# Performance work log

Measured on AMD Instinct MI355X. Metric: run time of the kernel, lower is better.

## Reference

```python
import jax, jax.numpy as jnp
import numpy as np

INPUT_DIM, PROJ_DIM, HIDDEN = 1, 16, 32
B, T = 2048, 2048


def setup_inputs() -> dict:
    key = jax.random.key(0)
    ks = jax.random.split(key, 9)
    s_in = 1.0 / np.sqrt(INPUT_DIM)
    s_h = 1.0 / np.sqrt(HIDDEN)
    s_p = 1.0 / np.sqrt(PROJ_DIM)
    return {
        "x_seq": jax.random.normal(ks[0], (B, T, INPUT_DIM), dtype=jnp.float32),
        # input_linear: Linear(input_dim, proj_dim)
        "Wp": jax.random.uniform(ks[1], (PROJ_DIM, INPUT_DIM), minval=-s_in, maxval=s_in),
        "bp": jax.random.uniform(ks[2], (PROJ_DIM,), minval=-s_in, maxval=s_in),
        # LSTM weights (PyTorch gate order i,f,g,o)
        "W_ih": jax.random.uniform(ks[3], (4 * HIDDEN, PROJ_DIM), minval=-s_h, maxval=s_h),
        "W_hh": jax.random.uniform(ks[4], (4 * HIDDEN, HIDDEN), minval=-s_h, maxval=s_h),
        "b_ih": jax.random.uniform(ks[5], (4 * HIDDEN,), minval=-s_h, maxval=s_h),
        "b_hh": jax.random.uniform(ks[6], (4 * HIDDEN,), minval=-s_h, maxval=s_h),
        # output_linear: Linear(hidden, input_dim)
        "Wo": jax.random.uniform(ks[7], (INPUT_DIM, HIDDEN), minval=-s_h, maxval=s_h),
        "bo": jax.random.uniform(ks[8], (INPUT_DIM,), minval=-s_h, maxval=s_h),
    }


def reference(x_seq, Wp, bp, W_ih, W_hh, b_ih, b_hh, Wo, bo):
    H = W_hh.shape[1]
    b, t, _ = x_seq.shape
    # input projection for all timesteps at once (same math as per-step Linear)
    # then pre-apply W_ih: [B,T,4H]
    xp = jnp.einsum("bti,pi->btp", x_seq, Wp) + bp
    gates_x = jnp.einsum("btp,gp->btg", xp, W_ih) + b_ih + b_hh
    gates_x = jnp.transpose(gates_x, (1, 0, 2))  # [T,B,4H]

    def step(carry, gx):
        h, c = carry
        gates = gx + h @ W_hh.T  # [B,4H]
        i, f, g, o = jnp.split(gates, 4, axis=-1)
        i = jax.nn.sigmoid(i)
        f = jax.nn.sigmoid(f)
        g = jnp.tanh(g)
        o = jax.nn.sigmoid(o)
        c = f * c + i * g
        h = o * jnp.tanh(c)
        return (h, c), h

    h0 = jnp.zeros((b, H), dtype=x_seq.dtype)
    c0 = jnp.zeros((b, H), dtype=x_seq.dtype)
    (_, _), hs = jax.lax.scan(step, (h0, c0), gates_x)  # hs: [T,B,H]
    outputs = jnp.einsum("tbh,oh->bto", hs, Wo) + bo  # [B,T,input_dim]
    return outputs
```

## Files before the change

kernel.cpp:

```cpp
#include <hip/hip_runtime.h>


#define BB 2048
#define TT 2048
#define HH 32

typedef _Float16 h2 __attribute__((ext_vector_type(2)));

__device__ __forceinline__ float gate_eval(float x, float m, float a, float b) {
    float e = __builtin_amdgcn_exp2f(x * m);
    float r = __builtin_amdgcn_rcpf(1.0f + e);
    return fmaf(a, r, b);
}

template <int CTRL>
__device__ __forceinline__ float dpp_add(float v) {
    int s = __builtin_amdgcn_update_dpp(0, __float_as_int(v), CTRL, 0xf, 0xf, true);
    return v + __int_as_float(s);
}

struct HVec { h2 v[16]; };

__device__ __forceinline__ HVec gather_h(const _Float16* base) {
    const float4* p = (const float4*)base;
    float4 q0 = p[0], q1 = p[1], q2 = p[2], q3 = p[3];
    HVec r;
    r.v[0]  = __builtin_bit_cast(h2, q0.x); r.v[1]  = __builtin_bit_cast(h2, q0.y);
    r.v[2]  = __builtin_bit_cast(h2, q0.z); r.v[3]  = __builtin_bit_cast(h2, q0.w);
    r.v[4]  = __builtin_bit_cast(h2, q1.x); r.v[5]  = __builtin_bit_cast(h2, q1.y);
    r.v[6]  = __builtin_bit_cast(h2, q1.z); r.v[7]  = __builtin_bit_cast(h2, q1.w);
    r.v[8]  = __builtin_bit_cast(h2, q2.x); r.v[9]  = __builtin_bit_cast(h2, q2.y);
    r.v[10] = __builtin_bit_cast(h2, q2.z); r.v[11] = __builtin_bit_cast(h2, q2.w);
    r.v[12] = __builtin_bit_cast(h2, q3.x); r.v[13] = __builtin_bit_cast(h2, q3.y);
    r.v[14] = __builtin_bit_cast(h2, q3.z); r.v[15] = __builtin_bit_cast(h2, q3.w);
    return r;
}

__global__ __launch_bounds__(256) void lstm_fused_kernel(
    const float* __restrict__ x_seq,
    const float* __restrict__ Wp,
    const float* __restrict__ bp,
    const float* __restrict__ W_ih,
    const float* __restrict__ W_hh,
    const float* __restrict__ b_ih,
    const float* __restrict__ b_hh,
    const float* __restrict__ Wo,
    const float* __restrict__ bo,
    float* __restrict__ out)
{
    const int tid  = threadIdx.x;
    const int wave = tid >> 6;
    const int lane = tid & 63;
    const int half = lane >> 5;
    const int j    = lane & 31;
    const int b    = blockIdx.x * 8 + wave * 2 + half;

    const int rI = j, rF = HH + j, rG = 2 * HH + j, rO = 3 * HH + j;

    h2 wI[16], wF[16], wG[16], wO[16];
    {
        const float2* pI = (const float2*)(W_hh + rI * HH);
        const float2* pF = (const float2*)(W_hh + rF * HH);
        const float2* pG = (const float2*)(W_hh + rG * HH);
        const float2* pO = (const float2*)(W_hh + rO * HH);
#pragma unroll
        for (int k = 0; k < 16; ++k) {
            float2 a = pI[k], f = pF[k], g = pG[k], o = pO[k];
            wI[k].x = (_Float16)a.x; wI[k].y = (_Float16)a.y;
            wF[k].x = (_Float16)f.x; wF[k].y = (_Float16)f.y;
            wG[k].x = (_Float16)g.x; wG[k].y = (_Float16)g.y;
            wO[k].x = (_Float16)o.x; wO[k].y = (_Float16)o.y;
        }
    }

    float aI = 0.f, cI = 0.f, aF = 0.f, cF = 0.f;
    float aG = 0.f, cG = 0.f, aO = 0.f, cO = 0.f;
#pragma unroll
    for (int p = 0; p < 16; ++p) {
        float wpv = Wp[p], bpv = bp[p];
        float wi = W_ih[rI * 16 + p], wf = W_ih[rF * 16 + p];
        float wg = W_ih[rG * 16 + p], wo_ = W_ih[rO * 16 + p];
        aI = fmaf(wi, wpv, aI);  cI = fmaf(wi, bpv, cI);
        aF = fmaf(wf, wpv, aF);  cF = fmaf(wf, bpv, cF);
        aG = fmaf(wg, wpv, aG);  cG = fmaf(wg, bpv, cG);
        aO = fmaf(wo_, wpv, aO); cO = fmaf(wo_, bpv, cO);
    }
    cI += b_ih[rI] + b_hh[rI];
    cF += b_ih[rF] + b_hh[rF];
    cG += b_ih[rG] + b_hh[rG];
    cO += b_ih[rO] + b_hh[rO];

    const float LOG2E = 1.44269504088896340736f;
    const float woj = Wo[j];
    const float bo0 = bo[0];

    __shared__ __align__(16) _Float16 hsh[4][2][HH];
    _Float16* hbase = &hsh[wave][half][0];
    hbase[j] = (_Float16)0.0f;

    float c = 0.0f;
    const float* xp = x_seq + (size_t)b * TT;
    float* op = out + (size_t)b * TT;

    HVec hcur = gather_h(hbase);
    float4 x4 = *(const float4*)(xp);

    for (int t = 0; t < TT; t += 4) {
        const int tn = (t + 4 < TT) ? (t + 4) : t;
        float4 x4n = *(const float4*)(xp + tn);
        float outv[4];
#pragma unroll
        for (int u = 0; u < 4; ++u) {
            float xv = (u == 0) ? x4.x : (u == 1) ? x4.y : (u == 2) ? x4.z : x4.w;

            float sI0 = cI, sI1 = xv * aI;
            float sF0 = cF, sF1 = xv * aF;
            float sG0 = cG, sG1 = xv * aG;
            float sO0 = cO, sO1 = xv * aO;
#pragma unroll
            for (int k = 0; k < 16; k += 2) {
                h2 h0 = hcur.v[k], h1 = hcur.v[k + 1];
                sI0 = __builtin_amdgcn_fdot2(wI[k],     h0, sI0, false);
                sF0 = __builtin_amdgcn_fdot2(wF[k],     h0, sF0, false);
                sG0 = __builtin_amdgcn_fdot2(wG[k],     h0, sG0, false);
                sO0 = __builtin_amdgcn_fdot2(wO[k],     h0, sO0, false);
                sI1 = __builtin_amdgcn_fdot2(wI[k + 1], h1, sI1, false);
                sF1 = __builtin_amdgcn_fdot2(wF[k + 1], h1, sF1, false);
                sG1 = __builtin_amdgcn_fdot2(wG[k + 1], h1, sG1, false);
                sO1 = __builtin_amdgcn_fdot2(wO[k + 1], h1, sO1, false);
            }

            float iv = gate_eval(sI0 + sI1, -LOG2E, 1.0f, 0.0f);
            float fv = gate_eval(sF0 + sF1, -LOG2E, 1.0f, 0.0f);
            float gv = gate_eval(sG0 + sG1, -2.0f * LOG2E, 2.0f, -1.0f);
            float ov = gate_eval(sO0 + sO1, -LOG2E, 1.0f, 0.0f);

            c = fmaf(fv, c, iv * gv);
            float th = gate_eval(c, -2.0f * LOG2E, 2.0f, -1.0f);
            float h = ov * th;

            hbase[j] = (_Float16)h;
            hcur = gather_h(hbase);

            float po = woj * h;
            po = dpp_add<0x111>(po);
            po = dpp_add<0x112>(po);
            po = dpp_add<0x114>(po);
            po = dpp_add<0x118>(po);
            po = dpp_add<0x142>(po);
            outv[u] = po + bo0;
        }
        if ((lane & 31) == 31) {
            *(float4*)(op + t) = make_float4(outv[0], outv[1], outv[2], outv[3]);
        }
        x4 = x4n;
    }
}

extern "C" void kernel_launch(void* const* d_in, const int* in_sizes, int n_in,
                              void* d_out, int out_size, void* d_ws, size_t ws_size,
                              hipStream_t stream) {
    const float* x_seq = (const float*)d_in[0];
    const float* Wp    = (const float*)d_in[1];
    const float* bp    = (const float*)d_in[2];
    const float* W_ih  = (const float*)d_in[3];
    const float* W_hh  = (const float*)d_in[4];
    const float* b_ih  = (const float*)d_in[5];
    const float* b_hh  = (const float*)d_in[6];
    const float* Wo    = (const float*)d_in[7];
    const float* bo    = (const float*)d_in[8];
    float* out = (float*)d_out;

    dim3 grid(BB / 8);
    dim3 block(256);
    lstm_fused_kernel<<<grid, block, 0, stream>>>(
        x_seq, Wp, bp, W_ih, W_hh, b_ih, b_hh, Wo, bo, out);
}
```

Before: 670.2 us.

## Replace LDS hidden-state broadcast with DPP/swizzle register exchange network

Each step now shares the hidden state between the 32 lanes with a ds_swizzle, a byte perm and a chain of DPP moves instead of writing to LDS and reading back 64 bytes. Lane j therefore holds a permuted set of h values. The recurrent weights are reloaded in the matching permuted order, using indices that run through the same network once at startup. This is meant to take LDS write/read latency off the serial per-timestep critical path, at the cost of about 16 dependent DPP ops, and it relies on the permutation being correct.

```diff
diff --git a/kernel.cpp b/kernel.cpp
--- a/kernel.cpp
+++ b/kernel.cpp
@@ -14,25 +14,40 @@
 }
 
 template <int CTRL>
+__device__ __forceinline__ int dpp_mov(int v) {
+    return __builtin_amdgcn_update_dpp(0, v, CTRL, 0xf, 0xf, true);
+}
+
+template <int CTRL>
 __device__ __forceinline__ float dpp_add(float v) {
     int s = __builtin_amdgcn_update_dpp(0, __float_as_int(v), CTRL, 0xf, 0xf, true);
     return v + __int_as_float(s);
 }
 
-struct HVec { h2 v[16]; };
+struct HVec { int v[16]; };
 
-__device__ __forceinline__ HVec gather_h(const _Float16* base) {
-    const float4* p = (const float4*)base;
-    float4 q0 = p[0], q1 = p[1], q2 = p[2], q3 = p[3];
+__device__ __forceinline__ HVec gather_net(float h) {
+    _Float16 hf = (_Float16)h;
+    unsigned hb = (unsigned)__builtin_bit_cast(unsigned short, hf);
+    int dup = (int)(hb | (hb << 16));
+    int prt = __builtin_amdgcn_ds_swizzle(dup, 0x401F);
     HVec r;
-    r.v[0]  = __builtin_bit_cast(h2, q0.x); r.v[1]  = __builtin_bit_cast(h2, q0.y);
-    r.v[2]  = __builtin_bit_cast(h2, q0.z); r.v[3]  = __builtin_bit_cast(h2, q0.w);
-    r.v[4]  = __builtin_bit_cast(h2, q1.x); r.v[5]  = __builtin_bit_cast(h2, q1.y);
-    r.v[6]  = __builtin_bit_cast(h2, q1.z); r.v[7]  = __builtin_bit_cast(h2, q1.w);
-    r.v[8]  = __builtin_bit_cast(h2, q2.x); r.v[9]  = __builtin_bit_cast(h2, q2.y);
-    r.v[10] = __builtin_bit_cast(h2, q2.z); r.v[11] = __builtin_bit_cast(h2, q2.w);
-    r.v[12] = __builtin_bit_cast(h2, q3.x); r.v[13] = __builtin_bit_cast(h2, q3.y);
-    r.v[14] = __builtin_bit_cast(h2, q3.z); r.v[15] = __builtin_bit_cast(h2, q3.w);
+    r.v[0] = (int)__builtin_amdgcn_perm((unsigned)prt, (unsigned)dup, 0x07060100u);
+    r.v[1] = dpp_mov<0xB1>(r.v[0]);
+    r.v[2] = dpp_mov<0x4E>(r.v[0]);
+    r.v[3] = dpp_mov<0x4E>(r.v[1]);
+    r.v[4] = dpp_mov<0x124>(r.v[0]);
+    r.v[5] = dpp_mov<0x124>(r.v[1]);
+    r.v[6] = dpp_mov<0x124>(r.v[2]);
+    r.v[7] = dpp_mov<0x124>(r.v[3]);
+    r.v[8]  = dpp_mov<0x128>(r.v[0]);
+    r.v[9]  = dpp_mov<0x128>(r.v[1]);
+    r.v[10] = dpp_mov<0x128>(r.v[2]);
+    r.v[11] = dpp_mov<0x128>(r.v[3]);
+    r.v[12] = dpp_mov<0x128>(r.v[4]);
+    r.v[13] = dpp_mov<0x128>(r.v[5]);
+    r.v[14] = dpp_mov<0x128>(r.v[6]);
+    r.v[15] = dpp_mov<0x128>(r.v[7]);
     return r;
 }
 
@@ -57,19 +72,22 @@
 
     const int rI = j, rF = HH + j, rG = 2 * HH + j, rO = 3 * HH + j;
 
+    HVec idx = gather_net((float)j);
     h2 wI[16], wF[16], wG[16], wO[16];
     {
-        const float2* pI = (const float2*)(W_hh + rI * HH);
-        const float2* pF = (const float2*)(W_hh + rF * HH);
-        const float2* pG = (const float2*)(W_hh + rG * HH);
-        const float2* pO = (const float2*)(W_hh + rO * HH);
+        const float* pI = W_hh + rI * HH;
+        const float* pF = W_hh + rF * HH;
+        const float* pG = W_hh + rG * HH;
+        const float* pO = W_hh + rO * HH;
 #pragma unroll
-        for (int k = 0; k < 16; ++k) {
-            float2 a = pI[k], f = pF[k], g = pG[k], o = pO[k];
-            wI[k].x = (_Float16)a.x; wI[k].y = (_Float16)a.y;
-            wF[k].x = (_Float16)f.x; wF[k].y = (_Float16)f.y;
-            wG[k].x = (_Float16)g.x; wG[k].y = (_Float16)g.y;
-            wO[k].x = (_Float16)o.x; wO[k].y = (_Float16)o.y;
+        for (int s = 0; s < 16; ++s) {
+            h2 iv = __builtin_bit_cast(h2, idx.v[s]);
+            int kx = (int)(float)iv.x;
+            int ky = (int)(float)iv.y;
+            wI[s].x = (_Float16)pI[kx]; wI[s].y = (_Float16)pI[ky];
+            wF[s].x = (_Float16)pF[kx]; wF[s].y = (_Float16)pF[ky];
+            wG[s].x = (_Float16)pG[kx]; wG[s].y = (_Float16)pG[ky];
+            wO[s].x = (_Float16)pO[kx]; wO[s].y = (_Float16)pO[ky];
         }
     }
 
@@ -94,15 +112,14 @@
     const float woj = Wo[j];
     const float bo0 = bo[0];
 
-    __shared__ __align__(16) _Float16 hsh[4][2][HH];
-    _Float16* hbase = &hsh[wave][half][0];
-    hbase[j] = (_Float16)0.0f;
-
     float c = 0.0f;
     const float* xp = x_seq + (size_t)b * TT;
     float* op = out + (size_t)b * TT;
 
-    HVec hcur = gather_h(hbase);
+    HVec hcur;
+#pragma unroll
+    for (int s = 0; s < 16; ++s) hcur.v[s] = 0;
+
     float4 x4 = *(const float4*)(xp);
 
     for (int t = 0; t < TT; t += 4) {
@@ -119,7 +136,8 @@
             float sO0 = cO, sO1 = xv * aO;
 #pragma unroll
             for (int k = 0; k < 16; k += 2) {
-                h2 h0 = hcur.v[k], h1 = hcur.v[k + 1];
+                h2 h0 = __builtin_bit_cast(h2, hcur.v[k]);
+                h2 h1 = __builtin_bit_cast(h2, hcur.v[k + 1]);
                 sI0 = __builtin_amdgcn_fdot2(wI[k],     h0, sI0, false);
                 sF0 = __builtin_amdgcn_fdot2(wF[k],     h0, sF0, false);
                 sG0 = __builtin_amdgcn_fdot2(wG[k],     h0, sG0, false);
@@ -139,8 +157,7 @@
             float th = gate_eval(c, -2.0f * LOG2E, 2.0f, -1.0f);
             float h = ov * th;
 
-            hbase[j] = (_Float16)h;
-            hcur = gather_h(hbase);
+            hcur = gather_net(h);
 
             float po = woj * h;
             po = dpp_add<0x111>(po);
```

Result: slower. 731.0 us (+9.1%).
